# Optimization experiments

Measured on AMD Instinct MI355X. Metric: run time of the kernel, lower is better.

The kernel has to match this reference:

```python
import jax, jax.numpy as jnp
import numpy as np

N = 30000        # nodes
E = 480000       # edges (before self-loops)
F_IN = 512       # input feature dim
HID = 64         # per-head hidden dim
HEADS = 4
WIDTH = HID * HEADS  # 256, concat heads
LAYERS = 3
NCLS = 40
NEG_SLOPE = 0.2


def setup_inputs() -> dict:
    key = jax.random.key(0)
    ks = jax.random.split(key, 16)
    def p(k, shape, scale=0.1):
        return jax.random.normal(k, shape, dtype=jnp.float32) * scale
    return {
        "x": jax.random.normal(ks[0], (N, F_IN), dtype=jnp.float32),
        "edge_index": jax.random.randint(ks[1], (2, E), 0, N, dtype=jnp.int32),
        # layer 1: F_IN -> HEADS*HID (concat)
        "W1": p(ks[2], (F_IN, WIDTH)), "as1": p(ks[3], (HEADS, HID)), "ad1": p(ks[4], (HEADS, HID)), "b1": p(ks[5], (WIDTH,)),
        # layer 2: WIDTH -> WIDTH
        "W2": p(ks[6], (WIDTH, WIDTH)), "as2": p(ks[7], (HEADS, HID)), "ad2": p(ks[8], (HEADS, HID)), "b2": p(ks[9], (WIDTH,)),
        # layer 3: WIDTH -> WIDTH
        "W3": p(ks[10], (WIDTH, WIDTH)), "as3": p(ks[11], (HEADS, HID)), "ad3": p(ks[12], (HEADS, HID)), "b3": p(ks[13], (WIDTH,)),
        # JK='cat' output head: WIDTH*LAYERS -> NCLS
        "Wo": p(ks[14], (WIDTH * LAYERS, NCLS)), "bo": p(ks[15], (NCLS,)),
    }


def gat_layer(x, Wm, a_src, a_dst, b, src, dst):
    # PyG GATConv (concat=True, eval mode): h = xW reshaped [N,H,C];
    # e_ij = leaky_relu(a_src.h_j + a_dst.h_i) for edge j->i, softmax over dst groups.
    n = x.shape[0]
    H, C = a_src.shape
    h = (x @ Wm).reshape(n, H, C)                      # [N,H,C]
    es = jnp.sum(h * a_src, axis=-1)                   # [N,H]
    ed = jnp.sum(h * a_dst, axis=-1)                   # [N,H]
    e = jax.nn.leaky_relu(es[src] + ed[dst], NEG_SLOPE)  # [Etot,H]
    m = jax.ops.segment_max(e, dst, num_segments=n)    # stable softmax per dst node
    w = jnp.exp(e - m[dst])
    den = jax.ops.segment_sum(w, dst, num_segments=n)
    alpha = w / den[dst]                               # [Etot,H]
    out = jax.ops.segment_sum(h[src] * alpha[:, :, None], dst, num_segments=n)  # [N,H,C]
    return out.reshape(n, H * C) + b


def reference(x, edge_index, W1, as1, ad1, b1, W2, as2, ad2, b2, W3, as3, ad3, b3, Wo, bo):
    # add self-loops (PyG GATConv default)
    loops = jnp.arange(N, dtype=edge_index.dtype)
    src = jnp.concatenate([edge_index[0], loops])
    dst = jnp.concatenate([edge_index[1], loops])
    # dropout is identity in eval mode
    h1 = jax.nn.relu(gat_layer(x, W1, as1, ad1, b1, src, dst))
    h2 = jax.nn.relu(gat_layer(h1, W2, as2, ad2, b2, src, dst))
    h3 = jax.nn.relu(gat_layer(h2, W3, as3, ad3, b3, src, dst))
    h = jnp.concatenate([h1, h2, h3], axis=-1)         # JK 'cat': [N, WIDTH*LAYERS]
    return h @ Wo + bo                                 # [N, NCLS]
```

## Files before the change

kernel.cpp:

```cpp
#include <hip/hip_runtime.h>

#define N_NODES 30000
#define N_EDGES 480000
#define ETOT    510000
#define F_IN    512
#define WIDTH   256
#define NCLS    40
#define KCAT    768
#define NPAD    48
#define TM      32
#define BROWS   272
#define HST     264

typedef __attribute__((ext_vector_type(8))) short short8;
typedef __attribute__((ext_vector_type(4))) float f32x4;

__device__ __forceinline__ unsigned short f2bf(float f){
  unsigned u = __float_as_uint(f);
  u += 0x7fffu + ((u >> 16) & 1u);
  return (unsigned short)(u >> 16);
}
__device__ __forceinline__ float b2f(unsigned short s){
  return __uint_as_float(((unsigned)s) << 16);
}

__device__ __forceinline__ void gload_lds16(const void* g, void* l){
  __builtin_amdgcn_global_load_lds(
      (const __attribute__((address_space(1))) unsigned int*)g,
      (__attribute__((address_space(3))) unsigned int*)l, 16, 0, 0);
}

__global__ void transpose_w_kernel(const float* __restrict__ W, unsigned short* __restrict__ Wt,
                                   int K, int Nc){
  int k = blockIdx.x * blockDim.x + threadIdx.x;
  int n = blockIdx.y;
  if (k < K) Wt[(size_t)n * K + k] = f2bf(W[(size_t)k * Nc + n]);
}

__global__ __launch_bounds__(256) void av_kernel(const float* __restrict__ W,
                                                 const float* __restrict__ a_s,
                                                 const float* __restrict__ a_d,
                                                 unsigned short* __restrict__ Bt, int K){
  int k = blockIdx.x;
  int tid = threadIdx.x;
  int h = tid >> 6, lane = tid & 63;
  float wv = W[(size_t)k * WIDTH + tid];
  float ps = wv * a_s[tid];
  float pd = wv * a_d[tid];
  #pragma unroll
  for (int off = 32; off; off >>= 1){
    ps += __shfl_down(ps, off, 64);
    pd += __shfl_down(pd, off, 64);
  }
  if (lane == 0){
    Bt[(size_t)(256 + h) * K + k] = f2bf(ps);
    Bt[(size_t)(260 + h) * K + k] = f2bf(pd);
  }
  if (tid < 8) Bt[(size_t)(264 + tid) * K + k] = 0;
}

__global__ void transpose_wo_kernel(const float* __restrict__ Wo, unsigned short* __restrict__ WoT){
  int i = blockIdx.x * blockDim.x + threadIdx.x;
  if (i < NPAD * KCAT){
    int c = i / KCAT, k = i - c * KCAT;
    WoT[i] = (c < NCLS) ? f2bf(Wo[(size_t)k * NCLS + c]) : (unsigned short)0;
  }
}

__global__ void zero_kernel(int* __restrict__ p, int n){
  int i = blockIdx.x * blockDim.x + threadIdx.x;
  if (i < n) p[i] = 0;
}

__global__ void hist_kernel(const int* __restrict__ ei, int* __restrict__ counts){
  int e = blockIdx.x * blockDim.x + threadIdx.x;
  if (e < ETOT){
    int d = (e < N_EDGES) ? ei[N_EDGES + e] : (e - N_EDGES);
    atomicAdd(&counts[d], 1);
  }
}

__global__ __launch_bounds__(1024) void scan_kernel(const int* __restrict__ counts,
                                                    int* __restrict__ offsets,
                                                    int* __restrict__ cursor, int n){
  __shared__ int wsum[16];
  int tid = threadIdx.x, lane = tid & 63, wid = tid >> 6;
  int running = 0;
  int nchunks = (n + 1023) >> 10;
  for (int ch = 0; ch < nchunks; ++ch){
    int i = (ch << 10) + tid;
    int v = (i < n) ? counts[i] : 0;
    int x = v;
    #pragma unroll
    for (int off = 1; off < 64; off <<= 1){
      int t = __shfl_up(x, off, 64);
      if (lane >= off) x += t;
    }
    if (lane == 63) wsum[wid] = x;
    __syncthreads();
    if (wid == 0){
      int s = (lane < 16) ? wsum[lane] : 0;
      #pragma unroll
      for (int off = 1; off < 16; off <<= 1){
        int t = __shfl_up(s, off, 64);
        if (lane >= off) s += t;
      }
      if (lane < 16) wsum[lane] = s;
    }
    __syncthreads();
    int waveprefix = (wid > 0) ? wsum[wid - 1] : 0;
    int excl = x - v + waveprefix + running;
    if (i < n){ offsets[i] = excl; cursor[i] = excl; }
    running += wsum[15];
    __syncthreads();
  }
  if (tid == 0) offsets[n] = running;
}

__global__ void scatter_kernel(const int* __restrict__ ei, int* __restrict__ cursor,
                               int* __restrict__ srcs){
  int e = blockIdx.x * blockDim.x + threadIdx.x;
  if (e < ETOT){
    int s, d;
    if (e < N_EDGES){ s = ei[e]; d = ei[N_EDGES + e]; }
    else { s = e - N_EDGES; d = s; }
    int pos = atomicAdd(&cursor[d], 1);
    srcs[pos] = s;
  }
}

template<int K, bool AF32>
__global__ __launch_bounds__(512, 4)
void gemm_bres_kernel(const void* __restrict__ Araw,
                      const unsigned short* __restrict__ Bt,
                      float* __restrict__ esd,
                      unsigned short* __restrict__ hb,
                      int M){
  constexpr int KT = K / 32;
  constexpr int NP = K / 256;
  constexpr int KTP = KT / NP;
  constexpr int KE = KT / 8;
  constexpr int ROWB = K * 2;
  __shared__ unsigned short Abuf[TM * K];
  __shared__ unsigned short hstage[TM * HST];
  __shared__ float cmbE[8][TM][9];

  int tid = threadIdx.x;
  int lane = tid & 63, w = tid >> 6;
  int l15 = lane & 15, quad = lane >> 4;
  int c0 = w * 32;
  int r0 = blockIdx.x * TM;

  uint4 va[8];
  if constexpr (AF32){
    const char* xb = (const char*)Araw;
    #pragma unroll
    for (int i = 0; i < 8; ++i){
      int L32 = (i * 512 + tid) * 16;
      int row = L32 >> 11;
      int colb = L32 & 2047;
      int grow = r0 + row; if (grow > M - 1) grow = M - 1;
      va[i] = *(const uint4*)(xb + (size_t)grow * 2048 + colb);
    }
  } else {
    const char* Ab = (const char*)Araw;
    #pragma unroll
    for (int c = 0; c < 2; ++c){
      int L = (c * 512 + tid) * 16;
      int row = L / ROWB;
      int colb = L % ROWB;
      int grow = r0 + row; if (grow > M - 1) grow = M - 1;
      gload_lds16(Ab + (size_t)grow * ROWB + (colb ^ ((row & 7) << 4)),
                  (char*)Abuf + L);
    }
  }

  short8 Bfe[KE];
  #pragma unroll
  for (int i = 0; i < KE; ++i){
    int kt = w * KE + i;
    Bfe[i] = *(const short8*)(Bt + (size_t)(256 + l15) * K + kt*32 + quad*8);
  }

  if constexpr (AF32){
    #pragma unroll
    for (int i = 0; i < 8; ++i){
      int ob = (i * 512 + tid) * 8;
      int row = ob >> 10;
      unsigned u0 = (unsigned)f2bf(__uint_as_float(va[i].x)) |
                    ((unsigned)f2bf(__uint_as_float(va[i].y)) << 16);
      unsigned u1 = (unsigned)f2bf(__uint_as_float(va[i].z)) |
                    ((unsigned)f2bf(__uint_as_float(va[i].w)) << 16);
      uint2 uv; uv.x = u0; uv.y = u1;
      *(uint2*)((char*)Abuf + (ob ^ ((row & 7) << 4))) = uv;
    }
  }
  __syncthreads();

  f32x4 acc[2][2];
  f32x4 eacc[2];
  #pragma unroll
  for (int s = 0; s < 2; ++s){
    acc[s][0] = (f32x4){0.f,0.f,0.f,0.f};
    acc[s][1] = (f32x4){0.f,0.f,0.f,0.f};
    eacc[s]   = (f32x4){0.f,0.f,0.f,0.f};
  }

  #pragma unroll 1
  for (int p = 0; p < NP; ++p){
    short8 Bf[KTP][2];
    #pragma unroll
    for (int kt2 = 0; kt2 < KTP; ++kt2){
      #pragma unroll
      for (int ct = 0; ct < 2; ++ct){
        Bf[kt2][ct] = *(const short8*)(Bt + (size_t)(c0 + ct*16 + l15) * K
                                          + (p*KTP + kt2)*32 + quad*8);
      }
    }
    __builtin_amdgcn_sched_barrier(0);
    #pragma unroll
    for (int s = 0; s < 2; ++s){
      int row = s * 16 + l15;
      int swzus = (row & 7) << 3;
      const unsigned short* base = Abuf + row * K;
      #pragma unroll
      for (int kt2 = 0; kt2 < KTP; ++kt2){
        int kofs = (p*KTP + kt2)*32 + quad*8;
        short8 af = *(const short8*)(base + (kofs ^ swzus));
        acc[s][0] = __builtin_amdgcn_mfma_f32_16x16x32_bf16(af, Bf[kt2][0], acc[s][0], 0, 0, 0);
        acc[s][1] = __builtin_amdgcn_mfma_f32_16x16x32_bf16(af, Bf[kt2][1], acc[s][1], 0, 0, 0);
      }
    }
  }

  #pragma unroll
  for (int s = 0; s < 2; ++s){
    int row = s * 16 + l15;
    int swzus = (row & 7) << 3;
    const unsigned short* base = Abuf + row * K;
    #pragma unroll
    for (int i = 0; i < KE; ++i){
      int kt = w * KE + i;
      short8 af = *(const short8*)(base + ((kt*32 + quad*8) ^ swzus));
      eacc[s] = __builtin_amdgcn_mfma_f32_16x16x32_bf16(af, Bfe[i], eacc[s], 0, 0, 0);
    }
  }

  #pragma unroll
  for (int s = 0; s < 2; ++s){
    #pragma unroll
    for (int r = 0; r < 4; ++r){
      int row = s * 16 + quad * 4 + r;
      hstage[row * HST + c0 + l15]      = f2bf(acc[s][0][r]);
      hstage[row * HST + c0 + 16 + l15] = f2bf(acc[s][1][r]);
      if (l15 < 8) cmbE[w][row][l15] = eacc[s][r];
    }
  }
  __syncthreads();

  #pragma unroll
  for (int p2 = 0; p2 < 2; ++p2){
    int us = (p2 * 512 + tid) * 8;
    int row = us >> 8, col = us & 255;
    if (r0 + row < M){
      uint4 v = *(const uint4*)(&hstage[row * HST + col]);
      *(uint4*)(hb + (size_t)(r0 + row) * WIDTH + col) = v;
    }
  }
  if (tid < 256){
    int row = tid >> 3, j = tid & 7;
    if (r0 + row < M){
      float v = 0.f;
      #pragma unroll
      for (int ww = 0; ww < 8; ++ww) v += cmbE[ww][row][j];
      esd[(size_t)(r0 + row) * 8 + j] = v;
    }
  }
}

__global__ __launch_bounds__(256) void agg_kernel(const int* __restrict__ offsets,
                                                  const int* __restrict__ srcs,
                                                  const float* __restrict__ esd,
                                                  const unsigned short* __restrict__ hb,
                                                  const float* __restrict__ bias,
                                                  unsigned short* __restrict__ hout){
  __shared__ float eLds[8][64][4];
  __shared__ int   sLds[8][64];
  int wid = threadIdx.x >> 6;
  int lane = threadIdx.x & 63;
  int half = lane >> 5, l32 = lane & 31;
  int slot = wid * 2 + half;
  int n = blockIdx.x * 8 + slot;
  int base = offsets[n];
  int deg = offsets[n + 1] - base;
  float4 edv = *(const float4*)(esd + (size_t)n * 8 + 4);

  float m0 = -1e30f, m1 = -1e30f, m2 = -1e30f, m3 = -1e30f;
  for (int i = l32; i < deg; i += 32){
    int s = srcs[base + i];
    float4 ev = *(const float4*)(esd + (size_t)s * 8);
    float e0 = ev.x + edv.x, e1 = ev.y + edv.y, e2 = ev.z + edv.z, e3 = ev.w + edv.w;
    e0 = e0 > 0.f ? e0 : 0.2f * e0;
    e1 = e1 > 0.f ? e1 : 0.2f * e1;
    e2 = e2 > 0.f ? e2 : 0.2f * e2;
    e3 = e3 > 0.f ? e3 : 0.2f * e3;
    if (i < 64){
      sLds[slot][i] = s;
      *(float4*)(&eLds[slot][i][0]) = (float4){e0, e1, e2, e3};
    }
    m0 = fmaxf(m0, e0); m1 = fmaxf(m1, e1); m2 = fmaxf(m2, e2); m3 = fmaxf(m3, e3);
  }
  #pragma unroll
  for (int off = 1; off < 32; off <<= 1){
    m0 = fmaxf(m0, __shfl_xor(m0, off, 64));
    m1 = fmaxf(m1, __shfl_xor(m1, off, 64));
    m2 = fmaxf(m2, __shfl_xor(m2, off, 64));
    m3 = fmaxf(m3, __shfl_xor(m3, off, 64));
  }
  int head = l32 >> 3;
  float mh  = (head == 0) ? m0 : (head == 1) ? m1 : (head == 2) ? m2 : m3;
  float edh = (head == 0) ? edv.x : (head == 1) ? edv.y : (head == 2) ? edv.z : edv.w;

  float2 a0 = {0.f,0.f}, a1 = {0.f,0.f}, a2 = {0.f,0.f}, a3 = {0.f,0.f};
  float den = 0.f;
  const unsigned short* hcol = hb + 8 * l32;
  for (int i = 0; i < deg; i += 8){
    int sidx[8]; float wgt[8];
    #pragma unroll
    for (int u = 0; u < 8; ++u){
      int idx = i + u;
      bool v = idx < deg;
      float le; int s;
      if (idx < 64 || !v){
        int ic = v ? idx : 0;
        if (ic >= 64) ic = 0;
        s  = sLds[slot][ic];
        le = eLds[slot][ic][head];
      } else {
        s = srcs[base + idx];
        float e = esd[(size_t)s * 8 + head] + edh;
        le = e > 0.f ? e : 0.2f * e;
      }
      sidx[u] = s;
      wgt[u] = v ? __expf(le - mh) : 0.f;
    }
    uint4 hv[8];
    #pragma unroll
    for (int u = 0; u < 8; ++u)
      hv[u] = *(const uint4*)(hcol + (size_t)sidx[u] * WIDTH);
    #pragma unroll
    for (int u = 0; u < 8; ++u){
      float wu = wgt[u];
      den += wu;
      a0.x += wu * __uint_as_float(hv[u].x << 16);
      a0.y += wu * __uint_as_float(hv[u].x & 0xffff0000u);
      a1.x += wu * __uint_as_float(hv[u].y << 16);
      a1.y += wu * __uint_as_float(hv[u].y & 0xffff0000u);
      a2.x += wu * __uint_as_float(hv[u].z << 16);
      a2.y += wu * __uint_as_float(hv[u].z & 0xffff0000u);
      a3.x += wu * __uint_as_float(hv[u].w << 16);
      a3.y += wu * __uint_as_float(hv[u].w & 0xffff0000u);
    }
  }
  float inv = 1.0f / den;
  const float* bp = bias + 8 * l32;
  float4 bv0 = *(const float4*)(bp);
  float4 bv1 = *(const float4*)(bp + 4);
  float o0 = fmaxf(a0.x * inv + bv0.x, 0.f);
  float o1 = fmaxf(a0.y * inv + bv0.y, 0.f);
  float o2 = fmaxf(a1.x * inv + bv0.z, 0.f);
  float o3 = fmaxf(a1.y * inv + bv0.w, 0.f);
  float o4 = fmaxf(a2.x * inv + bv1.x, 0.f);
  float o5 = fmaxf(a2.y * inv + bv1.y, 0.f);
  float o6 = fmaxf(a3.x * inv + bv1.z, 0.f);
  float o7 = fmaxf(a3.y * inv + bv1.w, 0.f);
  uint4 o;
  o.x = (unsigned)f2bf(o0) | ((unsigned)f2bf(o1) << 16);
  o.y = (unsigned)f2bf(o2) | ((unsigned)f2bf(o3) << 16);
  o.z = (unsigned)f2bf(o4) | ((unsigned)f2bf(o5) << 16);
  o.w = (unsigned)f2bf(o6) | ((unsigned)f2bf(o7) << 16);
  *(uint4*)(hout + (size_t)n * WIDTH + 8 * l32) = o;
}

__global__ __launch_bounds__(256) void out_gemm_kernel(const unsigned short* __restrict__ h1,
                                                       const unsigned short* __restrict__ h2,
                                                       const unsigned short* __restrict__ h3,
                                                       const unsigned short* __restrict__ WoT,
                                                       const float* __restrict__ bo,
                                                       float* __restrict__ out){
  int tid = threadIdx.x, lane = tid & 63, wid = tid >> 6;
  int l15 = lane & 15, quad = lane >> 4;
  int m0 = blockIdx.x * 64 + 16 * wid;

  f32x4 acc[3];
  #pragma unroll
  for (int t = 0; t < 3; ++t) acc[t] = (f32x4){0.f, 0.f, 0.f, 0.f};

  int arow = m0 + l15; if (arow >= N_NODES) arow = N_NODES - 1;

  #pragma unroll
  for (int part = 0; part < 3; ++part){
    const unsigned short* hp = (part == 0) ? h1 : (part == 1) ? h2 : h3;
    const unsigned short* ap = hp + (size_t)arow * WIDTH;
    #pragma unroll
    for (int k0 = 0; k0 < WIDTH; k0 += 32){
      short8 af = *(const short8*)(ap + k0 + quad * 8);
      int kk = part * WIDTH + k0;
      #pragma unroll
      for (int t = 0; t < 3; ++t){
        short8 bf = *(const short8*)(WoT + (size_t)(16 * t + l15) * KCAT + kk + quad * 8);
        acc[t] = __builtin_amdgcn_mfma_f32_16x16x32_bf16(af, bf, acc[t], 0, 0, 0);
      }
    }
  }

  int r0 = m0 + quad * 4;
  #pragma unroll
  for (int t = 0; t < 3; ++t){
    int col = 16 * t + l15;
    if (col < NCLS){
      float bc = bo[col];
      #pragma unroll
      for (int r = 0; r < 4; ++r){
        int grow = r0 + r;
        if (grow < N_NODES) out[(size_t)grow * NCLS + col] = acc[t][r] + bc;
      }
    }
  }
}

static inline size_t align256(size_t x){ return (x + 255) & ~(size_t)255; }

extern "C" void kernel_launch(void* const* d_in, const int* in_sizes, int n_in,
                              void* d_out, int out_size, void* d_ws, size_t ws_size,
                              hipStream_t stream) {
  const float* x   = (const float*)d_in[0];
  const int*   ei  = (const int*)  d_in[1];
  const float* W1  = (const float*)d_in[2];
  const float* as1 = (const float*)d_in[3];
  const float* ad1 = (const float*)d_in[4];
  const float* b1  = (const float*)d_in[5];
  const float* W2  = (const float*)d_in[6];
  const float* as2 = (const float*)d_in[7];
  const float* ad2 = (const float*)d_in[8];
  const float* b2  = (const float*)d_in[9];
  const float* W3  = (const float*)d_in[10];
  const float* as3 = (const float*)d_in[11];
  const float* ad3 = (const float*)d_in[12];
  const float* b3  = (const float*)d_in[13];
  const float* Wo  = (const float*)d_in[14];
  const float* bo  = (const float*)d_in[15];
  float* out = (float*)d_out;

  char* p = (char*)d_ws;
  auto take = [&](size_t bytes) -> char* { char* cur = p; p += align256(bytes); return cur; };

  unsigned short* Wt1   = (unsigned short*)take((size_t)BROWS * F_IN * 2);
  unsigned short* Wt2   = (unsigned short*)take((size_t)BROWS * WIDTH * 2);
  unsigned short* Wt3   = (unsigned short*)take((size_t)BROWS * WIDTH * 2);
  unsigned short* WoT   = (unsigned short*)take((size_t)NPAD * KCAT * 2);
  unsigned short* hs    = (unsigned short*)take((size_t)N_NODES * WIDTH * 2);
  float*          esd   = (float*)take((size_t)N_NODES * 8 * 4);
  unsigned short* h1b   = (unsigned short*)take((size_t)N_NODES * WIDTH * 2);
  unsigned short* h2b   = (unsigned short*)take((size_t)N_NODES * WIDTH * 2);
  unsigned short* h3b   = (unsigned short*)take((size_t)N_NODES * WIDTH * 2);
  int*            counts  = (int*)take((size_t)N_NODES * 4);
  int*            offsets = (int*)take((size_t)(N_NODES + 1) * 4);
  int*            cursor  = (int*)take((size_t)N_NODES * 4);
  int*            srcs    = (int*)take((size_t)ETOT * 4);

  transpose_w_kernel<<<dim3(F_IN / 256, WIDTH), 256, 0, stream>>>(W1, Wt1, F_IN, WIDTH);
  transpose_w_kernel<<<dim3(1, WIDTH), 256, 0, stream>>>(W2, Wt2, WIDTH, WIDTH);
  transpose_w_kernel<<<dim3(1, WIDTH), 256, 0, stream>>>(W3, Wt3, WIDTH, WIDTH);
  av_kernel<<<F_IN, 256, 0, stream>>>(W1, as1, ad1, Wt1, F_IN);
  av_kernel<<<WIDTH, 256, 0, stream>>>(W2, as2, ad2, Wt2, WIDTH);
  av_kernel<<<WIDTH, 256, 0, stream>>>(W3, as3, ad3, Wt3, WIDTH);
  transpose_wo_kernel<<<(NPAD * KCAT + 255) / 256, 256, 0, stream>>>(Wo, WoT);

  zero_kernel<<<(N_NODES + 255) / 256, 256, 0, stream>>>(counts, N_NODES);
  hist_kernel<<<(ETOT + 255) / 256, 256, 0, stream>>>(ei, counts);
  scan_kernel<<<1, 1024, 0, stream>>>(counts, offsets, cursor, N_NODES);
  scatter_kernel<<<(ETOT + 255) / 256, 256, 0, stream>>>(ei, cursor, srcs);

  const int ntiles = (N_NODES + TM - 1) / TM;
  const int agg_grid = N_NODES / 8;
  const int out_grid = (N_NODES + 63) / 64;

  gemm_bres_kernel<F_IN, true><<<ntiles, 512, 0, stream>>>(x, Wt1, esd, hs, N_NODES);
  agg_kernel<<<agg_grid, 256, 0, stream>>>(offsets, srcs, esd, hs, b1, h1b);
  gemm_bres_kernel<WIDTH, false><<<ntiles, 512, 0, stream>>>(h1b, Wt2, esd, hs, N_NODES);
  agg_kernel<<<agg_grid, 256, 0, stream>>>(offsets, srcs, esd, hs, b2, h2b);
  gemm_bres_kernel<WIDTH, false><<<ntiles, 512, 0, stream>>>(h2b, Wt3, esd, hs, N_NODES);
  agg_kernel<<<agg_grid, 256, 0, stream>>>(offsets, srcs, esd, hs, b3, h3b);

  out_gemm_kernel<<<out_grid, 256, 0, stream>>>(h1b, h2b, h3b, WoT, bo, out);
}
```

Before: 422.4 us.

## Fuse prep kernels, parallelize CSR scan, split es/ed arrays

Merges the weight transposes, attention-vector folding, Wo transpose and count zeroing into one prep kernel to cut launch count. The single-block sequential scan over 30000 counts becomes a three-kernel multi-block scan (partial, block-sum, add). The interleaved esd buffer is split into separate es and ed arrays so per-edge gathers in aggregation read a compact 16-byte stride. In exchange, the prep kernel branches on block index, and the multi-block scan adds two extra tiny launches.

```diff
diff --git a/kernel.cpp b/kernel.cpp
--- a/kernel.cpp
+++ b/kernel.cpp
@@ -30,18 +30,10 @@
       (__attribute__((address_space(3))) unsigned int*)l, 16, 0, 0);
 }
 
-__global__ void transpose_w_kernel(const float* __restrict__ W, unsigned short* __restrict__ Wt,
-                                   int K, int Nc){
-  int k = blockIdx.x * blockDim.x + threadIdx.x;
-  int n = blockIdx.y;
-  if (k < K) Wt[(size_t)n * K + k] = f2bf(W[(size_t)k * Nc + n]);
-}
-
-__global__ __launch_bounds__(256) void av_kernel(const float* __restrict__ W,
-                                                 const float* __restrict__ a_s,
-                                                 const float* __restrict__ a_d,
-                                                 unsigned short* __restrict__ Bt, int K){
-  int k = blockIdx.x;
+__device__ __forceinline__ void av_body(const float* __restrict__ W,
+                                        const float* __restrict__ a_s,
+                                        const float* __restrict__ a_d,
+                                        unsigned short* __restrict__ Bt, int K, int k){
   int tid = threadIdx.x;
   int h = tid >> 6, lane = tid & 63;
   float wv = W[(size_t)k * WIDTH + tid];
@@ -59,17 +51,45 @@
   if (tid < 8) Bt[(size_t)(264 + tid) * K + k] = 0;
 }
 
-__global__ void transpose_wo_kernel(const float* __restrict__ Wo, unsigned short* __restrict__ WoT){
-  int i = blockIdx.x * blockDim.x + threadIdx.x;
-  if (i < NPAD * KCAT){
+#define PREP_GRID (118 + 512 + 256 + 256 + 144 + 512 + 256 + 256)
+
+__global__ __launch_bounds__(256) void prep_kernel(
+    const float* __restrict__ W1, const float* __restrict__ as1, const float* __restrict__ ad1,
+    const float* __restrict__ W2, const float* __restrict__ as2, const float* __restrict__ ad2,
+    const float* __restrict__ W3, const float* __restrict__ as3, const float* __restrict__ ad3,
+    const float* __restrict__ Wo,
+    unsigned short* __restrict__ Wt1, unsigned short* __restrict__ Wt2,
+    unsigned short* __restrict__ Wt3, unsigned short* __restrict__ WoT,
+    int* __restrict__ counts){
+  int b = blockIdx.x, tid = threadIdx.x;
+  if (b < 118){
+    int i = b * 256 + tid;
+    if (i < N_NODES) counts[i] = 0;
+    return;
+  }
+  b -= 118;
+  if (b < 512){
+    int n = b >> 1, k = (b & 1) * 256 + tid;
+    Wt1[(size_t)n * F_IN + k] = f2bf(W1[(size_t)k * WIDTH + n]);
+    return;
+  }
+  b -= 512;
+  if (b < 256){ Wt2[(size_t)b * WIDTH + tid] = f2bf(W2[(size_t)tid * WIDTH + b]); return; }
+  b -= 256;
+  if (b < 256){ Wt3[(size_t)b * WIDTH + tid] = f2bf(W3[(size_t)tid * WIDTH + b]); return; }
+  b -= 256;
+  if (b < 144){
+    int i = b * 256 + tid;
     int c = i / KCAT, k = i - c * KCAT;
     WoT[i] = (c < NCLS) ? f2bf(Wo[(size_t)k * NCLS + c]) : (unsigned short)0;
-  }
-}
-
-__global__ void zero_kernel(int* __restrict__ p, int n){
-  int i = blockIdx.x * blockDim.x + threadIdx.x;
-  if (i < n) p[i] = 0;
+    return;
+  }
+  b -= 144;
+  if (b < 512){ av_body(W1, as1, ad1, Wt1, F_IN, b); return; }
+  b -= 512;
+  if (b < 256){ av_body(W2, as2, ad2, Wt2, WIDTH, b); return; }
+  b -= 256;
+  av_body(W3, as3, ad3, Wt3, WIDTH, b);
 }
 
 __global__ void hist_kernel(const int* __restrict__ ei, int* __restrict__ counts){
@@ -80,41 +100,60 @@
   }
 }
 
-__global__ __launch_bounds__(1024) void scan_kernel(const int* __restrict__ counts,
-                                                    int* __restrict__ offsets,
-                                                    int* __restrict__ cursor, int n){
+__global__ __launch_bounds__(1024) void scan_part_kernel(const int* __restrict__ counts,
+                                                         int* __restrict__ offsets,
+                                                         int* __restrict__ bsum, int n){
   __shared__ int wsum[16];
   int tid = threadIdx.x, lane = tid & 63, wid = tid >> 6;
-  int running = 0;
-  int nchunks = (n + 1023) >> 10;
-  for (int ch = 0; ch < nchunks; ++ch){
-    int i = (ch << 10) + tid;
-    int v = (i < n) ? counts[i] : 0;
-    int x = v;
-    #pragma unroll
-    for (int off = 1; off < 64; off <<= 1){
-      int t = __shfl_up(x, off, 64);
-      if (lane >= off) x += t;
-    }
-    if (lane == 63) wsum[wid] = x;
-    __syncthreads();
-    if (wid == 0){
-      int s = (lane < 16) ? wsum[lane] : 0;
-      #pragma unroll
-      for (int off = 1; off < 16; off <<= 1){
-        int t = __shfl_up(s, off, 64);
-        if (lane >= off) s += t;
-      }
-      if (lane < 16) wsum[lane] = s;
-    }
-    __syncthreads();
-    int waveprefix = (wid > 0) ? wsum[wid - 1] : 0;
-    int excl = x - v + waveprefix + running;
-    if (i < n){ offsets[i] = excl; cursor[i] = excl; }
-    running += wsum[15];
-    __syncthreads();
-  }
-  if (tid == 0) offsets[n] = running;
+  int i = blockIdx.x * 1024 + tid;
+  int v = (i < n) ? counts[i] : 0;
+  int x = v;
+  #pragma unroll
+  for (int off = 1; off < 64; off <<= 1){
+    int t = __shfl_up(x, off, 64);
+    if (lane >= off) x += t;
+  }
+  if (lane == 63) wsum[wid] = x;
+  __syncthreads();
+  if (wid == 0){
+    int s = (lane < 16) ? wsum[lane] : 0;
+    #pragma unroll
+    for (int off = 1; off < 16; off <<= 1){
+      int t = __shfl_up(s, off, 64);
+      if (lane >= off) s += t;
+    }
+    if (lane < 16) wsum[lane] = s;
+  }
+  __syncthreads();
+  int wp = (wid > 0) ? wsum[wid - 1] : 0;
+  if (i < n) offsets[i] = x - v + wp;
+  if (tid == 0) bsum[blockIdx.x] = wsum[15];
+}
+
+__global__ __launch_bounds__(64) void scan_bsum_kernel(int* __restrict__ bsum,
+                                                       int* __restrict__ offsets,
+                                                       int nb, int n){
+  int lane = threadIdx.x;
+  int v = (lane < nb) ? bsum[lane] : 0;
+  int x = v;
+  #pragma unroll
+  for (int off = 1; off < 64; off <<= 1){
+    int t = __shfl_up(x, off, 64);
+    if (lane >= off) x += t;
+  }
+  if (lane < nb) bsum[lane] = x - v;
+  if (lane == nb - 1) offsets[n] = x;
+}
+
+__global__ __launch_bounds__(1024) void scan_add_kernel(int* __restrict__ offsets,
+                                                        int* __restrict__ cursor,
+                                                        const int* __restrict__ bsum, int n){
+  int i = blockIdx.x * 1024 + threadIdx.x;
+  if (i < n){
+    int o = offsets[i] + bsum[blockIdx.x];
+    offsets[i] = o;
+    cursor[i] = o;
+  }
 }
 
 __global__ void scatter_kernel(const int* __restrict__ ei, int* __restrict__ cursor,
@@ -133,7 +172,8 @@
 __global__ __launch_bounds__(512, 4)
 void gemm_bres_kernel(const void* __restrict__ Araw,
                       const unsigned short* __restrict__ Bt,
-                      float* __restrict__ esd,
+                      float* __restrict__ es,
+                      float* __restrict__ ed,
                       unsigned short* __restrict__ hb,
                       int M){
   constexpr int KT = K / 32;
@@ -273,14 +313,16 @@
       float v = 0.f;
       #pragma unroll
       for (int ww = 0; ww < 8; ++ww) v += cmbE[ww][row][j];
-      esd[(size_t)(r0 + row) * 8 + j] = v;
+      if (j < 4) es[(size_t)(r0 + row) * 4 + j] = v;
+      else       ed[(size_t)(r0 + row) * 4 + (j - 4)] = v;
     }
   }
 }
 
 __global__ __launch_bounds__(256) void agg_kernel(const int* __restrict__ offsets,
                                                   const int* __restrict__ srcs,
-                                                  const float* __restrict__ esd,
+                                                  const float* __restrict__ es,
+                                                  const float* __restrict__ ed,
                                                   const unsigned short* __restrict__ hb,
                                                   const float* __restrict__ bias,
                                                   unsigned short* __restrict__ hout){
@@ -293,12 +335,12 @@
   int n = blockIdx.x * 8 + slot;
   int base = offsets[n];
   int deg = offsets[n + 1] - base;
-  float4 edv = *(const float4*)(esd + (size_t)n * 8 + 4);
+  float4 edv = *(const float4*)(ed + (size_t)n * 4);
 
   float m0 = -1e30f, m1 = -1e30f, m2 = -1e30f, m3 = -1e30f;
   for (int i = l32; i < deg; i += 32){
     int s = srcs[base + i];
-    float4 ev = *(const float4*)(esd + (size_t)s * 8);
+    float4 ev = *(const float4*)(es + (size_t)s * 4);
     float e0 = ev.x + edv.x, e1 = ev.y + edv.y, e2 = ev.z + edv.z, e3 = ev.w + edv.w;
     e0 = e0 > 0.f ? e0 : 0.2f * e0;
     e1 = e1 > 0.f ? e1 : 0.2f * e1;
@@ -338,7 +380,7 @@
         le = eLds[slot][ic][head];
       } else {
         s = srcs[base + idx];
-        float e = esd[(size_t)s * 8 + head] + edh;
+        float e = es[(size_t)s * 4 + head] + edh;
         le = e > 0.f ? e : 0.2f * e;
       }
       sidx[u] = s;
@@ -460,7 +502,8 @@
   unsigned short* Wt3   = (unsigned short*)take((size_t)BROWS * WIDTH * 2);
   unsigned short* WoT   = (unsigned short*)take((size_t)NPAD * KCAT * 2);
   unsigned short* hs    = (unsigned short*)take((size_t)N_NODES * WIDTH * 2);
-  float*          esd   = (float*)take((size_t)N_NODES * 8 * 4);
+  float*          es    = (float*)take((size_t)N_NODES * 4 * 4);
+  float*          ed    = (float*)take((size_t)N_NODES * 4 * 4);
   unsigned short* h1b   = (unsigned short*)take((size_t)N_NODES * WIDTH * 2);
   unsigned short* h2b   = (unsigned short*)take((size_t)N_NODES * WIDTH * 2);
   unsigned short* h3b   = (unsigned short*)take((size_t)N_NODES * WIDTH * 2);
@@ -468,30 +511,29 @@
   int*            offsets = (int*)take((size_t)(N_NODES + 1) * 4);
   int*            cursor  = (int*)take((size_t)N_NODES * 4);
   int*            srcs    = (int*)take((size_t)ETOT * 4);
-
-  transpose_w_kernel<<<dim3(F_IN / 256, WIDTH), 256, 0, stream>>>(W1, Wt1, F_IN, WIDTH);
-  transpose_w_kernel<<<dim3(1, WIDTH), 256, 0, stream>>>(W2, Wt2, WIDTH, WIDTH);
-  transpose_w_kernel<<<dim3(1, WIDTH), 256, 0, stream>>>(W3, Wt3, WIDTH, WIDTH);
-  av_kernel<<<F_IN, 256, 0, stream>>>(W1, as1, ad1, Wt1, F_IN);
-  av_kernel<<<WIDTH, 256, 0, stream>>>(W2, as2, ad2, Wt2, WIDTH);
-  av_kernel<<<WIDTH, 256, 0, stream>>>(W3, as3, ad3, Wt3, WIDTH);
-  transpose_wo_kernel<<<(NPAD * KCAT + 255) / 256, 256, 0, stream>>>(Wo, WoT);
-
-  zero_kernel<<<(N_NODES + 255) / 256, 256, 0, stream>>>(counts, N_NODES);
+  int*            bsum    = (int*)take((size_t)64 * 4);
+
+  prep_kernel<<<PREP_GRID, 256, 0, stream>>>(W1, as1, ad1, W2, as2, ad2,
+                                             W3, as3, ad3, Wo,
+                                             Wt1, Wt2, Wt3, WoT, counts);
+
+  const int nb = (N_NODES + 1023) / 1024;
   hist_kernel<<<(ETOT + 255) / 256, 256, 0, stream>>>(ei, counts);
-  scan_kernel<<<1, 1024, 0, stream>>>(counts, offsets, cursor, N_NODES);
+  scan_part_kernel<<<nb, 1024, 0, stream>>>(counts, offsets, bsum, N_NODES);
+  scan_bsum_kernel<<<1, 64, 0, stream>>>(bsum, offsets, nb, N_NODES);
+  scan_add_kernel<<<nb, 1024, 0, stream>>>(offsets, cursor, bsum, N_NODES);
   scatter_kernel<<<(ETOT + 255) / 256, 256, 0, stream>>>(ei, cursor, srcs);
 
   const int ntiles = (N_NODES + TM - 1) / TM;
   const int agg_grid = N_NODES / 8;
   const int out_grid = (N_NODES + 63) / 64;
 
-  gemm_bres_kernel<F_IN, true><<<ntiles, 512, 0, stream>>>(x, Wt1, esd, hs, N_NODES);
-  agg_kernel<<<agg_grid, 256, 0, stream>>>(offsets, srcs, esd, hs, b1, h1b);
-  gemm_bres_kernel<WIDTH, false><<<ntiles, 512, 0, stream>>>(h1b, Wt2, esd, hs, N_NODES);
-  agg_kernel<<<agg_grid, 256, 0, stream>>>(offsets, srcs, esd, hs, b2, h2b);
-  gemm_bres_kernel<WIDTH, false><<<ntiles, 512, 0, stream>>>(h2b, Wt3, esd, hs, N_NODES);
-  agg_kernel<<<agg_grid, 256, 0, stream>>>(offsets, srcs, esd, hs, b3, h3b);
+  gemm_bres_kernel<F_IN, true><<<ntiles, 512, 0, stream>>>(x, Wt1, es, ed, hs, N_NODES);
+  agg_kernel<<<agg_grid, 256, 0, stream>>>(offsets, srcs, es, ed, hs, b1, h1b);
+  gemm_bres_kernel<WIDTH, false><<<ntiles, 512, 0, stream>>>(h1b, Wt2, es, ed, hs, N_NODES);
+  agg_kernel<<<agg_grid, 256, 0, stream>>>(offsets, srcs, es, ed, hs, b2, h2b);
+  gemm_bres_kernel<WIDTH, false><<<ntiles, 512, 0, stream>>>(h2b, Wt3, es, ed, hs, N_NODES);
+  agg_kernel<<<agg_grid, 256, 0, stream>>>(offsets, srcs, es, ed, hs, b3, h3b);
 
   out_gemm_kernel<<<out_grid, 256, 0, stream>>>(h1b, h2b, h3b, WoT, bo, out);
 }
```

New measurement: 385.0 us. 8.9% less time.
